# Performance work log

Hardware: AMD Instinct MI355X
Metric: run time of the kernel (lower is better)

Reference implementation:

```python
import jax, jax.numpy as jnp
import numpy as np

N_BATCH, N_SEQ, N_CHANNELS = 32, 4096, 128
N_EXPERTS, TOP_K = 64, 2
D_IN = 2 * N_SEQ  # linear input width


def setup_inputs() -> dict:
    key = jax.random.key(0)
    k_x, k_wm, k_bm, k_wn, k_bn = jax.random.split(key, 5)
    scale = 1.0 / np.sqrt(D_IN)  # torch nn.Linear default init range
    return {
        "x": jax.random.normal(k_x, (N_BATCH, N_SEQ, N_CHANNELS, 2), dtype=jnp.float32),
        "W_main": jax.random.uniform(k_wm, (N_EXPERTS, D_IN), jnp.float32, -scale, scale),
        "b_main": jax.random.uniform(k_bm, (N_EXPERTS,), jnp.float32, -scale, scale),
        "W_noise": jax.random.uniform(k_wn, (N_EXPERTS, D_IN), jnp.float32, -scale, scale),
        "b_noise": jax.random.uniform(k_bn, (N_EXPERTS,), jnp.float32, -scale, scale),
    }


def _keep_top_k(logits, k):
    # torch.kthvalue(x, n-k) = (n-k)-th smallest (1-based) = sorted[:, n-k-1]
    n = logits.shape[1]
    if n < k:
        return logits
    kth = jnp.sort(logits, axis=1)[:, n - k - 1:n - k]  # [rows, 1]
    return jnp.where(logits > kth, logits, -jnp.inf)


def reference(x, W_main, b_main, W_noise, b_noise):
    n_batch, n_seq, n_channels, _ = x.shape
    # swapaxes(1,2) then reshape -> rows=[batch*channels], feat=[seq*2]
    x_r = jnp.swapaxes(x, 1, 2).reshape(n_batch * n_channels, 2 * n_seq)
    main_out = x_r @ W_main.T + b_main                      # [rows, E]
    noise_out = jax.nn.softplus(x_r @ W_noise.T + b_noise)  # [rows, E]
    gate = _keep_top_k(main_out + noise_out, TOP_K)
    return jax.nn.softmax(gate, axis=1)
```

## Files before the change

### kernel.cpp

```cpp
#include <hip/hip_runtime.h>
#include <cmath>

typedef _Float16 f16x8 __attribute__((ext_vector_type(8)));
typedef _Float16 f16x4 __attribute__((ext_vector_type(4)));
typedef float    f32x16 __attribute__((ext_vector_type(16)));

constexpr int NBATCH = 32;
constexpr int NSEQ   = 4096;
constexpr int NCH    = 128;
constexpr int NEXP   = 64;
constexpr int NE2    = 128;
constexpr int DIN    = 2 * NSEQ;
constexpr int ROWS   = NBATCH * NCH;
constexpr int KCH    = 16;
constexpr int KT     = 16;
constexpr float LOSC = 2048.0f;
constexpr float INV_LOSC = 1.0f / 2048.0f;

constexpr size_t WS_WHI = 32ull << 20;
constexpr size_t WS_WLO = 34ull << 20;

__device__ __forceinline__ int swz_f16(int row, int g) {
    return row * 32 + ((g ^ ((row >> 1) & 3)) << 3);
}

__device__ __forceinline__ void gload_lds16(const void* g, void* l) {
    __builtin_amdgcn_global_load_lds(
        (const __attribute__((address_space(1))) unsigned int*)g,
        (__attribute__((address_space(3))) unsigned int*)l, 16, 0, 0);
}

__global__ __launch_bounds__(256)
void wprep_kernel(const float* __restrict__ Wm, const float* __restrict__ Wn,
                  _Float16* __restrict__ Whi, _Float16* __restrict__ Wlo)
{
    const int idx = (blockIdx.x * 256 + threadIdx.x) * 4;
    const int row = idx >> 13;
    const int f   = idx & 8191;
    const float* src = (row < NEXP) ? (Wm + (size_t)row * DIN + f)
                                    : (Wn + (size_t)(row - NEXP) * DIN + f);
    const float4 v = *(const float4*)src;
    const int g  = (f >> 3) & 3;
    const int fs = (f & ~0x18) | ((g ^ ((row >> 1) & 3)) << 3);
    float vv[4] = { v.x, v.y, v.z, v.w };
    f16x4 h, l;
#pragma unroll
    for (int j = 0; j < 4; ++j) {
        _Float16 hj = (_Float16)vv[j];
        h[j] = hj;
        l[j] = (_Float16)((vv[j] - (float)hj) * LOSC);
    }
    *(f16x4*)&Whi[(size_t)row * 8192 + fs] = h;
    *(f16x4*)&Wlo[(size_t)row * 8192 + fs] = l;
}

__global__ __launch_bounds__(256, 2)
void gemm_kernel(const float* __restrict__ x,
                 const _Float16* __restrict__ Whi,
                 const _Float16* __restrict__ Wlo,
                 float* __restrict__ partials)
{
    const int l    = blockIdx.x;
    const int slot = l >> 3;
    const int kc   = (l & 7) + 8 * (slot & 1);
    const int b    = slot >> 1;

    const int tid  = threadIdx.x;
    const int lane = tid & 63;
    const int wave = tid >> 6;
    const int wm   = wave >> 1;
    const int wn   = wave & 1;

    __shared__ _Float16 lds[2 * 16384];

    f32x16 acc1[2][2], acc2[2][2];
#pragma unroll
    for (int mi = 0; mi < 2; ++mi)
#pragma unroll
        for (int ni = 0; ni < 2; ++ni)
#pragma unroll
            for (int r = 0; r < 16; ++r) { acc1[mi][ni][r] = 0.f; acc2[mi][ni][r] = 0.f; }

    const float* xchunk = x + (size_t)b * (NSEQ * 256) + (size_t)kc * (256 * 256);
    const int c    = tid & 127;
    const int gsel = tid >> 7;
    const int fb0  = kc * 512;
    const int e_ld = lane >> 2;
    const int goff = (lane & 3) * 8;

    float2 xr[2][8];

    auto load_x = [&](int t, float2 (&dst)[8]) {
#pragma unroll
        for (int u = 0; u < 2; ++u) {
            const int g = u * 2 + gsel;
#pragma unroll
            for (int i = 0; i < 4; ++i)
                dst[u * 4 + i] = *(const float2*)(xchunk + (size_t)(t * 16 + g * 4 + i) * 256 + c * 2);
        }
    };
    auto write_x = [&](int buf, float2 (&src)[8]) {
        _Float16* Ah = lds + buf * 16384;
        _Float16* Al = Ah + 4096;
#pragma unroll
        for (int u = 0; u < 2; ++u) {
            const int g = u * 2 + gsel;
            f16x8 h, lo;
#pragma unroll
            for (int i = 0; i < 4; ++i) {
                float a0 = src[u * 4 + i].x, a1 = src[u * 4 + i].y;
                _Float16 h0 = (_Float16)a0, h1 = (_Float16)a1;
                h[2 * i] = h0; h[2 * i + 1] = h1;
                lo[2 * i]     = (_Float16)((a0 - (float)h0) * LOSC);
                lo[2 * i + 1] = (_Float16)((a1 - (float)h1) * LOSC);
            }
            const int off = swz_f16(c, g);
            *(f16x8*)&Ah[off] = h;
            *(f16x8*)&Al[off] = lo;
        }
    };
    auto issue_W = [&](int t, int buf) {
        const int fb = fb0 + t * 32;
        _Float16* Bh = lds + buf * 16384 + 8192;
        _Float16* Bl = Bh + 4096;
#pragma unroll
        for (int q = 0; q < 2; ++q) {
            const int e0 = wave * 32 + q * 16;
            gload_lds16(Whi + (size_t)(e0 + e_ld) * 8192 + fb + goff, Bh + e0 * 32);
            gload_lds16(Wlo + (size_t)(e0 + e_ld) * 8192 + fb + goff, Bl + e0 * 32);
        }
    };

    issue_W(0, 0);
    load_x(0, xr[0]);
    load_x(1, xr[1]);
    write_x(0, xr[0]);
    asm volatile("s_waitcnt lgkmcnt(0)" ::: "memory");
    __builtin_amdgcn_s_barrier();
    __builtin_amdgcn_sched_barrier(0);

#pragma unroll
    for (int t = 0; t < KT; ++t) {
        const int buf = t & 1;

        if (t + 1 < KT) issue_W(t + 1, buf ^ 1);
        if (t + 2 < KT) load_x(t + 2, xr[buf]);
        __builtin_amdgcn_sched_barrier(0);

        const _Float16* Ah = lds + buf * 16384;
        const _Float16* Al = Ah + 4096;
        const _Float16* Bh = Ah + 8192;
        const _Float16* Bl = Ah + 12288;
#pragma unroll
        for (int kk = 0; kk < 2; ++kk) {
            const int gk = kk * 2 + (lane >> 5);
            f16x8 ah[2], al[2], bh[2], bl[2];
#pragma unroll
            for (int i = 0; i < 2; ++i) {
                const int oa = swz_f16(wm * 64 + i * 32 + (lane & 31), gk);
                const int ob = swz_f16(wn * 64 + i * 32 + (lane & 31), gk);
                ah[i] = *(const f16x8*)&Ah[oa];
                al[i] = *(const f16x8*)&Al[oa];
                bh[i] = *(const f16x8*)&Bh[ob];
                bl[i] = *(const f16x8*)&Bl[ob];
            }
#pragma unroll
            for (int mi = 0; mi < 2; ++mi)
#pragma unroll
                for (int ni = 0; ni < 2; ++ni) {
                    acc1[mi][ni] = __builtin_amdgcn_mfma_f32_32x32x16_f16(ah[mi], bh[ni], acc1[mi][ni], 0, 0, 0);
                    acc2[mi][ni] = __builtin_amdgcn_mfma_f32_32x32x16_f16(ah[mi], bl[ni], acc2[mi][ni], 0, 0, 0);
                    acc2[mi][ni] = __builtin_amdgcn_mfma_f32_32x32x16_f16(al[mi], bh[ni], acc2[mi][ni], 0, 0, 0);
                }
        }

        if (t + 1 < KT) {
            write_x(buf ^ 1, xr[buf ^ 1]);
            if (t + 2 < KT) asm volatile("s_waitcnt vmcnt(8) lgkmcnt(0)" ::: "memory");
            else            asm volatile("s_waitcnt vmcnt(0) lgkmcnt(0)" ::: "memory");
            __builtin_amdgcn_s_barrier();
            __builtin_amdgcn_sched_barrier(0);
        }
    }

    float* outp = partials + ((size_t)kc * ROWS + (size_t)b * NCH) * NE2;
#pragma unroll
    for (int mi = 0; mi < 2; ++mi)
#pragma unroll
        for (int ni = 0; ni < 2; ++ni)
#pragma unroll
            for (int r = 0; r < 16; ++r) {
                const int rloc = (r & 3) + 8 * (r >> 2) + 4 * (lane >> 5);
                const int crow = wm * 64 + mi * 32 + rloc;
                const int e    = wn * 64 + ni * 32 + (lane & 31);
                outp[(size_t)crow * NE2 + e] = acc1[mi][ni][r] + acc2[mi][ni][r] * INV_LOSC;
            }
}

__global__ __launch_bounds__(256)
void gate_kernel(const float* __restrict__ partials,
                 const float* __restrict__ bm,
                 const float* __restrict__ bn,
                 float* __restrict__ out)
{
    const int tid  = threadIdx.x;
    const int rl   = tid >> 7;
    const int e    = tid & 127;
    const int lane = tid & 63;
    const int row  = blockIdx.x * 2 + rl;

    const float* p = partials + (size_t)row * NE2 + e;
    float s = 0.f;
#pragma unroll
    for (int kc = 0; kc < KCH; ++kc)
        s += p[(size_t)kc * ROWS * NE2];

    __shared__ float spl[2][64];
    if (e >= NEXP) {
        float nz = s + bn[lane];
        spl[rl][lane] = fmaxf(nz, 0.f) + log1pf(expf(-fabsf(nz)));
    }
    __syncthreads();
    if (e < NEXP) {
        float g = s + bm[lane] + spl[rl][lane];

        float v  = g;
        float m1 = v;
#pragma unroll
        for (int o = 32; o > 0; o >>= 1) m1 = fmaxf(m1, __shfl_xor(m1, o));
        unsigned long long b1 = __ballot(v == m1);
        int l1 = __ffsll(b1) - 1;
        if (lane == l1) v = -INFINITY;
        float m2 = v;
#pragma unroll
        for (int o = 32; o > 0; o >>= 1) m2 = fmaxf(m2, __shfl_xor(m2, o));
        unsigned long long b2 = __ballot(v == m2);
        int l2 = __ffsll(b2) - 1;
        if (lane == l2) v = -INFINITY;
        float kth = v;
#pragma unroll
        for (int o = 32; o > 0; o >>= 1) kth = fmaxf(kth, __shfl_xor(kth, o));

        float ev  = (g > kth) ? expf(g - m1) : 0.f;
        float den = ev;
#pragma unroll
        for (int o = 32; o > 0; o >>= 1) den += __shfl_xor(den, o);
        out[(size_t)row * NEXP + lane] = ev / den;
    }
}

extern "C" void kernel_launch(void* const* d_in, const int* in_sizes, int n_in,
                              void* d_out, int out_size, void* d_ws, size_t ws_size,
                              hipStream_t stream)
{
    const float* x  = (const float*)d_in[0];
    const float* Wm = (const float*)d_in[1];
    const float* bm = (const float*)d_in[2];
    const float* Wn = (const float*)d_in[3];
    const float* bn = (const float*)d_in[4];
    float* out      = (float*)d_out;

    float*     partials = (float*)d_ws;
    _Float16*  Whi      = (_Float16*)((char*)d_ws + WS_WHI);
    _Float16*  Wlo      = (_Float16*)((char*)d_ws + WS_WLO);

    wprep_kernel<<<1024, 256, 0, stream>>>(Wm, Wn, Whi, Wlo);
    gemm_kernel<<<512, 256, 0, stream>>>(x, Whi, Wlo, partials);
    gate_kernel<<<ROWS / 2, 256, 0, stream>>>(partials, bm, bn, out);
}
```

Baseline: 211.4 us.

## Retile GEMM to 64-row blocks with longer K chunks and fewer partials

Each GEMM block now covers 64 channel rows instead of 128, while its K-chunk doubles (8 chunks of 32 tiles instead of 16 of 16). Per-wave accumulators shrink to two 32x32 tiles, and the main loop is restructured with a peeled tail and partial unroll. The aim is lower register pressure and LDS use, better occupancy, and half as much partial-sum traffic for the gate reduction. The trade-off is that W tiles are reloaded by twice as many row blocks, which adds W bandwidth and lowers MFMA reuse per LDS load. The gate kernel's KCH loop also shrinks automatically.

```diff
diff --git a/kernel.cpp b/kernel.cpp
--- a/kernel.cpp
+++ b/kernel.cpp
@@ -12,8 +12,8 @@
 constexpr int NE2    = 128;
 constexpr int DIN    = 2 * NSEQ;
 constexpr int ROWS   = NBATCH * NCH;
-constexpr int KCH    = 16;
-constexpr int KT     = 16;
+constexpr int KCH    = 8;
+constexpr int KT     = 32;
 constexpr float LOSC = 2048.0f;
 constexpr float INV_LOSC = 1.0f / 2048.0f;
 
@@ -60,68 +60,60 @@
                  const _Float16* __restrict__ Wlo,
                  float* __restrict__ partials)
 {
-    const int l    = blockIdx.x;
-    const int slot = l >> 3;
-    const int kc   = (l & 7) + 8 * (slot & 1);
-    const int b    = slot >> 1;
+    const int l  = blockIdx.x;
+    const int kc = l & 7;
+    const int rt = l >> 3;
+    const int b  = rt >> 1;
+    const int ch = rt & 1;
 
     const int tid  = threadIdx.x;
     const int lane = tid & 63;
     const int wave = tid >> 6;
-    const int wm   = wave >> 1;
-    const int wn   = wave & 1;
-
-    __shared__ _Float16 lds[2 * 16384];
-
-    f32x16 acc1[2][2], acc2[2][2];
-#pragma unroll
-    for (int mi = 0; mi < 2; ++mi)
-#pragma unroll
-        for (int ni = 0; ni < 2; ++ni)
-#pragma unroll
-            for (int r = 0; r < 16; ++r) { acc1[mi][ni][r] = 0.f; acc2[mi][ni][r] = 0.f; }
-
-    const float* xchunk = x + (size_t)b * (NSEQ * 256) + (size_t)kc * (256 * 256);
-    const int c    = tid & 127;
-    const int gsel = tid >> 7;
-    const int fb0  = kc * 512;
+    const int wm   = wave & 1;
+    const int wn   = wave >> 1;
+
+    __shared__ _Float16 lds[2 * 12288];
+
+    f32x16 acc1[2], acc2[2];
+#pragma unroll
+    for (int ni = 0; ni < 2; ++ni)
+#pragma unroll
+        for (int r = 0; r < 16; ++r) { acc1[ni][r] = 0.f; acc2[ni][r] = 0.f; }
+
+    const float* xchunk = x + (size_t)b * (NSEQ * 256) + (size_t)kc * (512 * 256) + ch * 128;
+    const int cl  = tid & 63;
+    const int pg  = tid >> 6;
+    const int fb0 = kc * 1024;
+
     const int e_ld = lane >> 2;
     const int goff = (lane & 3) * 8;
 
-    float2 xr[2][8];
-
-    auto load_x = [&](int t, float2 (&dst)[8]) {
-#pragma unroll
-        for (int u = 0; u < 2; ++u) {
-            const int g = u * 2 + gsel;
-#pragma unroll
-            for (int i = 0; i < 4; ++i)
-                dst[u * 4 + i] = *(const float2*)(xchunk + (size_t)(t * 16 + g * 4 + i) * 256 + c * 2);
-        }
-    };
-    auto write_x = [&](int buf, float2 (&src)[8]) {
-        _Float16* Ah = lds + buf * 16384;
-        _Float16* Al = Ah + 4096;
-#pragma unroll
-        for (int u = 0; u < 2; ++u) {
-            const int g = u * 2 + gsel;
-            f16x8 h, lo;
-#pragma unroll
-            for (int i = 0; i < 4; ++i) {
-                float a0 = src[u * 4 + i].x, a1 = src[u * 4 + i].y;
-                _Float16 h0 = (_Float16)a0, h1 = (_Float16)a1;
-                h[2 * i] = h0; h[2 * i + 1] = h1;
-                lo[2 * i]     = (_Float16)((a0 - (float)h0) * LOSC);
-                lo[2 * i + 1] = (_Float16)((a1 - (float)h1) * LOSC);
-            }
-            const int off = swz_f16(c, g);
-            *(f16x8*)&Ah[off] = h;
-            *(f16x8*)&Al[off] = lo;
-        }
+    float2 xr[2][4];
+
+    auto load_x = [&](int t, float2 (&dst)[4]) {
+#pragma unroll
+        for (int i = 0; i < 4; ++i)
+            dst[i] = *(const float2*)(xchunk + (size_t)(t * 16 + pg * 4 + i) * 256 + cl * 2);
+    };
+    auto write_x = [&](int buf, float2 (&src)[4]) {
+        _Float16* Ah = lds + buf * 12288;
+        _Float16* Al = Ah + 2048;
+        f16x8 h, lo;
+#pragma unroll
+        for (int i = 0; i < 4; ++i) {
+            float a0 = src[i].x, a1 = src[i].y;
+            _Float16 h0 = (_Float16)a0, h1 = (_Float16)a1;
+            h[2 * i] = h0; h[2 * i + 1] = h1;
+            lo[2 * i]     = (_Float16)((a0 - (float)h0) * LOSC);
+            lo[2 * i + 1] = (_Float16)((a1 - (float)h1) * LOSC);
+        }
+        const int off = swz_f16(cl, pg);
+        *(f16x8*)&Ah[off] = h;
+        *(f16x8*)&Al[off] = lo;
     };
     auto issue_W = [&](int t, int buf) {
         const int fb = fb0 + t * 32;
-        _Float16* Bh = lds + buf * 16384 + 8192;
+        _Float16* Bh = lds + buf * 12288 + 4096;
         _Float16* Bl = Bh + 4096;
 #pragma unroll
         for (int q = 0; q < 2; ++q) {
@@ -130,71 +122,70 @@
             gload_lds16(Wlo + (size_t)(e0 + e_ld) * 8192 + fb + goff, Bl + e0 * 32);
         }
     };
+    auto mfma_tile = [&](int buf) {
+        const _Float16* Ah = lds + buf * 12288;
+        const _Float16* Al = Ah + 2048;
+        const _Float16* Bh = Ah + 4096;
+        const _Float16* Bl = Ah + 8192;
+#pragma unroll
+        for (int kk = 0; kk < 2; ++kk) {
+            const int gk = kk * 2 + (lane >> 5);
+            const int oa = swz_f16(wm * 32 + (lane & 31), gk);
+            f16x8 ah = *(const f16x8*)&Ah[oa];
+            f16x8 al = *(const f16x8*)&Al[oa];
+#pragma unroll
+            for (int ni = 0; ni < 2; ++ni) {
+                const int ob = swz_f16(wn * 64 + ni * 32 + (lane & 31), gk);
+                f16x8 bh = *(const f16x8*)&Bh[ob];
+                f16x8 bl = *(const f16x8*)&Bl[ob];
+                acc1[ni] = __builtin_amdgcn_mfma_f32_32x32x16_f16(ah, bh, acc1[ni], 0, 0, 0);
+                acc2[ni] = __builtin_amdgcn_mfma_f32_32x32x16_f16(ah, bl, acc2[ni], 0, 0, 0);
+                acc2[ni] = __builtin_amdgcn_mfma_f32_32x32x16_f16(al, bh, acc2[ni], 0, 0, 0);
+            }
+        }
+    };
 
     issue_W(0, 0);
+    __builtin_amdgcn_sched_barrier(0);
     load_x(0, xr[0]);
     load_x(1, xr[1]);
+    __builtin_amdgcn_sched_barrier(0);
     write_x(0, xr[0]);
-    asm volatile("s_waitcnt lgkmcnt(0)" ::: "memory");
+    asm volatile("s_waitcnt vmcnt(4) lgkmcnt(0)" ::: "memory");
     __builtin_amdgcn_s_barrier();
     __builtin_amdgcn_sched_barrier(0);
 
-#pragma unroll
-    for (int t = 0; t < KT; ++t) {
-        const int buf = t & 1;
-
-        if (t + 1 < KT) issue_W(t + 1, buf ^ 1);
-        if (t + 2 < KT) load_x(t + 2, xr[buf]);
+#pragma unroll 2
+    for (int t = 0; t < KT - 2; ++t) {
+        const int cur = t & 1;
+        issue_W(t + 1, cur ^ 1);
         __builtin_amdgcn_sched_barrier(0);
-
-        const _Float16* Ah = lds + buf * 16384;
-        const _Float16* Al = Ah + 4096;
-        const _Float16* Bh = Ah + 8192;
-        const _Float16* Bl = Ah + 12288;
-#pragma unroll
-        for (int kk = 0; kk < 2; ++kk) {
-            const int gk = kk * 2 + (lane >> 5);
-            f16x8 ah[2], al[2], bh[2], bl[2];
-#pragma unroll
-            for (int i = 0; i < 2; ++i) {
-                const int oa = swz_f16(wm * 64 + i * 32 + (lane & 31), gk);
-                const int ob = swz_f16(wn * 64 + i * 32 + (lane & 31), gk);
-                ah[i] = *(const f16x8*)&Ah[oa];
-                al[i] = *(const f16x8*)&Al[oa];
-                bh[i] = *(const f16x8*)&Bh[ob];
-                bl[i] = *(const f16x8*)&Bl[ob];
-            }
-#pragma unroll
-            for (int mi = 0; mi < 2; ++mi)
-#pragma unroll
-                for (int ni = 0; ni < 2; ++ni) {
-                    acc1[mi][ni] = __builtin_amdgcn_mfma_f32_32x32x16_f16(ah[mi], bh[ni], acc1[mi][ni], 0, 0, 0);
-                    acc2[mi][ni] = __builtin_amdgcn_mfma_f32_32x32x16_f16(ah[mi], bl[ni], acc2[mi][ni], 0, 0, 0);
-                    acc2[mi][ni] = __builtin_amdgcn_mfma_f32_32x32x16_f16(al[mi], bh[ni], acc2[mi][ni], 0, 0, 0);
-                }
-        }
-
-        if (t + 1 < KT) {
-            write_x(buf ^ 1, xr[buf ^ 1]);
-            if (t + 2 < KT) asm volatile("s_waitcnt vmcnt(8) lgkmcnt(0)" ::: "memory");
-            else            asm volatile("s_waitcnt vmcnt(0) lgkmcnt(0)" ::: "memory");
-            __builtin_amdgcn_s_barrier();
-            __builtin_amdgcn_sched_barrier(0);
-        }
-    }
-
-    float* outp = partials + ((size_t)kc * ROWS + (size_t)b * NCH) * NE2;
-#pragma unroll
-    for (int mi = 0; mi < 2; ++mi)
-#pragma unroll
-        for (int ni = 0; ni < 2; ++ni)
-#pragma unroll
-            for (int r = 0; r < 16; ++r) {
-                const int rloc = (r & 3) + 8 * (r >> 2) + 4 * (lane >> 5);
-                const int crow = wm * 64 + mi * 32 + rloc;
-                const int e    = wn * 64 + ni * 32 + (lane & 31);
-                outp[(size_t)crow * NE2 + e] = acc1[mi][ni][r] + acc2[mi][ni][r] * INV_LOSC;
-            }
+        load_x(t + 2, xr[cur]);
+        __builtin_amdgcn_sched_barrier(0);
+        mfma_tile(cur);
+        write_x(cur ^ 1, xr[cur ^ 1]);
+        asm volatile("s_waitcnt vmcnt(4) lgkmcnt(0)" ::: "memory");
+        __builtin_amdgcn_s_barrier();
+        __builtin_amdgcn_sched_barrier(0);
+    }
+    issue_W(KT - 1, 1);
+    __builtin_amdgcn_sched_barrier(0);
+    mfma_tile(0);
+    write_x(1, xr[1]);
+    asm volatile("s_waitcnt vmcnt(0) lgkmcnt(0)" ::: "memory");
+    __builtin_amdgcn_s_barrier();
+    mfma_tile(1);
+
+    float* outp = partials + ((size_t)kc * ROWS + (size_t)b * NCH + ch * 64) * NE2;
+#pragma unroll
+    for (int ni = 0; ni < 2; ++ni)
+#pragma unroll
+        for (int r = 0; r < 16; ++r) {
+            const int rloc = (r & 3) + 8 * (r >> 2) + 4 * (lane >> 5);
+            const int crow = wm * 32 + rloc;
+            const int e    = wn * 64 + ni * 32 + (lane & 31);
+            outp[(size_t)crow * NE2 + e] = acc1[ni][r] + acc2[ni][r] * INV_LOSC;
+        }
 }
 
 __global__ __launch_bounds__(256)
```

After: 221.3 us. 4.7% more time.
